# Kernel optimization log

Measured on AMD Instinct MI355X. Metric: run time of the kernel, lower is better.

The kernel has to match this reference:

```python
import jax, jax.numpy as jnp
import numpy as np

N, DIM, HEADS = 4096, 256, 4
DK = DIM // HEADS
EPS = 1e-5


def setup_inputs() -> dict:
    key = jax.random.key(0)
    ks = jax.random.split(key, 12)
    x = jax.random.normal(ks[0], (N, DIM), dtype=jnp.float32)
    adj = (jax.random.uniform(ks[1], (N, N)) < 0.05).astype(jnp.float32)
    s = 1.0 / np.sqrt(DIM).astype(np.float32)
    Wq = jax.random.normal(ks[2], (DIM, DIM), dtype=jnp.float32) * s
    bq = jnp.zeros((DIM,), jnp.float32)
    Wk = jax.random.normal(ks[3], (DIM, DIM), dtype=jnp.float32) * s
    bk = jnp.zeros((DIM,), jnp.float32)
    Wv = jax.random.normal(ks[4], (DIM, DIM), dtype=jnp.float32) * s
    bv = jnp.zeros((DIM,), jnp.float32)
    Wo = jax.random.normal(ks[5], (DIM, DIM), dtype=jnp.float32) * s
    bo = jnp.zeros((DIM,), jnp.float32)
    gamma = jnp.ones((DIM,), jnp.float32)
    beta = jnp.zeros((DIM,), jnp.float32)
    return {"x": x, "adj": adj, "Wq": Wq, "bq": bq, "Wk": Wk, "bk": bk,
            "Wv": Wv, "bv": bv, "Wo": Wo, "bo": bo, "gamma": gamma, "beta": beta}


def reference(x, adj, Wq, bq, Wk, bk, Wv, bv, Wo, bo, gamma, beta):
    n = x.shape[0]
    # projections -> [N, H, dk]
    Q = (x @ Wq.T + bq).reshape(n, HEADS, DK)
    K = (x @ Wk.T + bk).reshape(n, HEADS, DK)
    V = (x @ Wv.T + bv).reshape(n, HEADS, DK)
    inv_sqrt_dk = jnp.asarray(1.0 / np.sqrt(DK), x.dtype)
    # [N, N, H] scores, multiplicative adjacency mask BEFORE softmax
    scores = jnp.einsum('ihd,jhd->ijh', Q, K) * inv_sqrt_dk
    scores = scores * adj[:, :, None]
    weights = jax.nn.softmax(scores, axis=1)  # softmax over source nodes j
    out = jnp.einsum('ijh,jhd->ihd', weights, V).reshape(n, DIM)
    out = out @ Wo.T + bo
    # residual + LayerNorm
    h = out + x
    mu = jnp.mean(h, axis=-1, keepdims=True)
    var = jnp.mean(jnp.square(h - mu), axis=-1, keepdims=True)
    return (h - mu) * jax.lax.rsqrt(var + EPS) * gamma + beta
```

## Files before the change

### kernel.cpp

```cpp
#include <hip/hip_runtime.h>
#include <math.h>

#define NN 4096
#define ECAP 768

typedef float f32x4 __attribute__((ext_vector_type(4)));

__device__ __forceinline__ float bf2f(unsigned short u) {
    union { unsigned int i; float f; } c; c.i = ((unsigned int)u) << 16; return c.f;
}
__device__ __forceinline__ unsigned short f2bf(float f) {
    union { float f; unsigned int i; } c; c.f = f;
    const unsigned int r = c.i + 0x7FFFu + ((c.i >> 16) & 1u);
    return (unsigned short)(r >> 16);
}

__global__ __launch_bounds__(256) void qkv_gemm(
    const float* __restrict__ x,
    const float* __restrict__ Wq, const float* __restrict__ Wk, const float* __restrict__ Wv,
    const float* __restrict__ bq, const float* __restrict__ bk, const float* __restrict__ bv,
    float* __restrict__ Q, unsigned short* __restrict__ Kb, unsigned short* __restrict__ Vb,
    float* __restrict__ S)
{
    __shared__ float As[32][68];
    __shared__ float Bs[32][68];

    const int which = blockIdx.z;
    const float* __restrict__ W    = which == 0 ? Wq : (which == 1 ? Wk : Wv);
    const float* __restrict__ bias = which == 0 ? bq : (which == 1 ? bk : bv);

    const int tid = threadIdx.x;
    const int tx = tid & 15, ty = tid >> 4;
    const int row0 = blockIdx.x * 64, col0 = blockIdx.y * 64;
    const int lr = tid >> 3;
    const int lc = (tid & 7) * 4;

    float acc[4][4] = {};

    for (int k0 = 0; k0 < 256; k0 += 32) {
        const float4 a0 = *(const float4*)(x + (size_t)(row0 + lr) * 256 + k0 + lc);
        const float4 a1 = *(const float4*)(x + (size_t)(row0 + lr + 32) * 256 + k0 + lc);
        const float4 w0 = *(const float4*)(W + (size_t)(col0 + lr) * 256 + k0 + lc);
        const float4 w1 = *(const float4*)(W + (size_t)(col0 + lr + 32) * 256 + k0 + lc);
        __syncthreads();
        As[lc + 0][lr] = a0.x; As[lc + 1][lr] = a0.y; As[lc + 2][lr] = a0.z; As[lc + 3][lr] = a0.w;
        As[lc + 0][lr + 32] = a1.x; As[lc + 1][lr + 32] = a1.y; As[lc + 2][lr + 32] = a1.z; As[lc + 3][lr + 32] = a1.w;
        Bs[lc + 0][lr] = w0.x; Bs[lc + 1][lr] = w0.y; Bs[lc + 2][lr] = w0.z; Bs[lc + 3][lr] = w0.w;
        Bs[lc + 0][lr + 32] = w1.x; Bs[lc + 1][lr + 32] = w1.y; Bs[lc + 2][lr + 32] = w1.z; Bs[lc + 3][lr + 32] = w1.w;
        __syncthreads();
#pragma unroll
        for (int kk = 0; kk < 32; kk++) {
            const float4 av = *(const float4*)&As[kk][ty * 4];
            const float4 bv4 = *(const float4*)&Bs[kk][tx * 4];
            acc[0][0] = fmaf(av.x, bv4.x, acc[0][0]); acc[0][1] = fmaf(av.x, bv4.y, acc[0][1]);
            acc[0][2] = fmaf(av.x, bv4.z, acc[0][2]); acc[0][3] = fmaf(av.x, bv4.w, acc[0][3]);
            acc[1][0] = fmaf(av.y, bv4.x, acc[1][0]); acc[1][1] = fmaf(av.y, bv4.y, acc[1][1]);
            acc[1][2] = fmaf(av.y, bv4.z, acc[1][2]); acc[1][3] = fmaf(av.y, bv4.w, acc[1][3]);
            acc[2][0] = fmaf(av.z, bv4.x, acc[2][0]); acc[2][1] = fmaf(av.z, bv4.y, acc[2][1]);
            acc[2][2] = fmaf(av.z, bv4.z, acc[2][2]); acc[2][3] = fmaf(av.z, bv4.w, acc[2][3]);
            acc[3][0] = fmaf(av.w, bv4.x, acc[3][0]); acc[3][1] = fmaf(av.w, bv4.y, acc[3][1]);
            acc[3][2] = fmaf(av.w, bv4.z, acc[3][2]); acc[3][3] = fmaf(av.w, bv4.w, acc[3][3]);
        }
    }

    const int gc = col0 + tx * 4;
    const float4 b4 = *(const float4*)(bias + gc);
    float cs0 = 0.f, cs1 = 0.f, cs2 = 0.f, cs3 = 0.f;
#pragma unroll
    for (int r = 0; r < 4; r++) {
        const int gr = row0 + ty * 4 + r;
        float4 v;
        v.x = acc[r][0] + b4.x; v.y = acc[r][1] + b4.y;
        v.z = acc[r][2] + b4.z; v.w = acc[r][3] + b4.w;
        if (which == 0) {
            *(float4*)(Q + (size_t)gr * 256 + gc) = v;
        } else {
            ushort4 pk;
            pk.x = f2bf(v.x); pk.y = f2bf(v.y); pk.z = f2bf(v.z); pk.w = f2bf(v.w);
            *(ushort4*)((which == 1 ? Kb : Vb) + (size_t)gr * 256 + gc) = pk;
            cs0 += v.x; cs1 += v.y; cs2 += v.z; cs3 += v.w;
        }
    }
    if (which == 2) {
        __syncthreads();
        float* red = &As[0][0];
        red[ty * 68 + tx * 4 + 0] = cs0;
        red[ty * 68 + tx * 4 + 1] = cs1;
        red[ty * 68 + tx * 4 + 2] = cs2;
        red[ty * 68 + tx * 4 + 3] = cs3;
        __syncthreads();
        if (ty == 0) {
#pragma unroll
            for (int c = 0; c < 4; c++) {
                float s = 0.f;
#pragma unroll
                for (int t = 0; t < 16; t++) s += red[t * 68 + tx * 4 + c];
                atomicAdd(&S[gc + c], s);
            }
        }
    }
}

__global__ __launch_bounds__(512, 4) void attn_v4(
    const float* __restrict__ Q, const unsigned short* __restrict__ K,
    const unsigned short* __restrict__ V, const float* __restrict__ adj,
    const float* __restrict__ S, float* __restrict__ out)
{
    __shared__ unsigned short lj[ECAP];
    __shared__ float wgt[ECAP * 4];
    __shared__ float pnum[2][256];
    __shared__ float pden[2][4];
    __shared__ int wtot[8], wbase[8], cnt;

    const int i = blockIdx.x;
    const int tid = threadIdx.x;
    const int wave = tid >> 6;
    const int lane = tid & 63;

    const f32x4* __restrict__ arow = (const f32x4*)(adj + (size_t)i * NN);
    const f32x4 a0 = __builtin_nontemporal_load(arow + 2 * tid);
    const f32x4 a1 = __builtin_nontemporal_load(arow + 2 * tid + 1);
    const int c = (a0.x != 0.f) + (a0.y != 0.f) + (a0.z != 0.f) + (a0.w != 0.f)
                + (a1.x != 0.f) + (a1.y != 0.f) + (a1.z != 0.f) + (a1.w != 0.f);
    int incl = c;
#pragma unroll
    for (int s = 1; s < 64; s <<= 1) {
        const int v = __shfl_up(incl, s);
        if (lane >= s) incl += v;
    }
    if (lane == 63) wtot[wave] = incl;
    __syncthreads();
    if (tid == 0) {
        int s = 0;
#pragma unroll
        for (int w = 0; w < 8; w++) { wbase[w] = s; s += wtot[w]; }
        cnt = s;
    }
    __syncthreads();
    {
        int p = wbase[wave] + incl - c;
        const int j0 = tid * 8;
        if (a0.x != 0.f && p < ECAP) lj[p++] = (unsigned short)(j0 + 0);
        if (a0.y != 0.f && p < ECAP) lj[p++] = (unsigned short)(j0 + 1);
        if (a0.z != 0.f && p < ECAP) lj[p++] = (unsigned short)(j0 + 2);
        if (a0.w != 0.f && p < ECAP) lj[p++] = (unsigned short)(j0 + 3);
        if (a1.x != 0.f && p < ECAP) lj[p++] = (unsigned short)(j0 + 4);
        if (a1.y != 0.f && p < ECAP) lj[p++] = (unsigned short)(j0 + 5);
        if (a1.z != 0.f && p < ECAP) lj[p++] = (unsigned short)(j0 + 6);
        if (a1.w != 0.f && p < ECAP) lj[p++] = (unsigned short)(j0 + 7);
    }
    __syncthreads();
    const int m = min(cnt, ECAP);

    const float4 qraw = ((const float4*)(Q + (size_t)i * 256))[lane];
    const float QS = 0.125f * 1.44269504089f;
    const float4 qv = {qraw.x * QS, qraw.y * QS, qraw.z * QS, qraw.w * QS};
    for (int e0 = wave * 4; e0 < m; e0 += 32) {
        int jj[4];
#pragma unroll
        for (int u = 0; u < 4; u++)
            jj[u] = (e0 + u < m) ? (int)lj[e0 + u] : (int)lj[e0];
        ushort4 kv[4];
#pragma unroll
        for (int u = 0; u < 4; u++)
            kv[u] = ((const ushort4*)(K + (size_t)jj[u] * 256))[lane];
#pragma unroll
        for (int u = 0; u < 4; u++) {
            float d = bf2f(kv[u].x) * qv.x + bf2f(kv[u].y) * qv.y
                    + bf2f(kv[u].z) * qv.z + bf2f(kv[u].w) * qv.w;
            d += __shfl_xor(d, 1);
            d += __shfl_xor(d, 2);
            d += __shfl_xor(d, 4);
            d += __shfl_xor(d, 8);
            if ((lane & 15) == 0 && e0 + u < m)
                wgt[(e0 + u) * 4 + (lane >> 4)] = exp2f(d) - 1.f;
        }
    }
    __syncthreads();

    const int g = tid >> 8;
    const int d = tid & 255;
    const int head = d >> 6;
    float num = 0.f, den = 0.f;
    int e = g;
    for (; e + 14 < m; e += 16) {
        float w[8];
#pragma unroll
        for (int u = 0; u < 8; u++) w[u] = wgt[(e + 2 * u) * 4 + head];
        float v[8];
#pragma unroll
        for (int u = 0; u < 8; u++)
            v[u] = bf2f(V[(size_t)lj[e + 2 * u] * 256 + d]);
#pragma unroll
        for (int u = 0; u < 8; u++) { num = fmaf(w[u], v[u], num); den += w[u]; }
    }
    for (; e < m; e += 2) {
        const float w = wgt[e * 4 + head];
        num = fmaf(w, bf2f(V[(size_t)lj[e] * 256 + d]), num);
        den += w;
    }
    pnum[g][d] = num;
    if ((d & 63) == 0) pden[g][head] = den;
    __syncthreads();

    if (tid < 256) {
        const int h = tid >> 6;
        const float dn = pden[0][h] + pden[1][h] + 4096.0f;
        out[(size_t)i * 256 + tid] = (pnum[0][tid] + pnum[1][tid] + S[tid]) / dn;
    }
}

__global__ __launch_bounds__(256) void out_gemm(
    const float* __restrict__ A, const float* __restrict__ Wo,
    const float* __restrict__ bo, const float* __restrict__ x,
    float* __restrict__ H)
{
    __shared__ float As[32][68];
    __shared__ float Bs[32][68];
    const int tid = threadIdx.x;
    const int tx = tid & 15, ty = tid >> 4;
    const int row0 = blockIdx.x * 64, col0 = blockIdx.y * 64;
    const int lr = tid >> 3;
    const int lc = (tid & 7) * 4;

    float acc[4][4] = {};

    for (int k0 = 0; k0 < 256; k0 += 32) {
        const float4 a0 = *(const float4*)(A + (size_t)(row0 + lr) * 256 + k0 + lc);
        const float4 a1 = *(const float4*)(A + (size_t)(row0 + lr + 32) * 256 + k0 + lc);
        const float4 w0 = *(const float4*)(Wo + (size_t)(col0 + lr) * 256 + k0 + lc);
        const float4 w1 = *(const float4*)(Wo + (size_t)(col0 + lr + 32) * 256 + k0 + lc);
        __syncthreads();
        As[lc + 0][lr] = a0.x; As[lc + 1][lr] = a0.y; As[lc + 2][lr] = a0.z; As[lc + 3][lr] = a0.w;
        As[lc + 0][lr + 32] = a1.x; As[lc + 1][lr + 32] = a1.y; As[lc + 2][lr + 32] = a1.z; As[lc + 3][lr + 32] = a1.w;
        Bs[lc + 0][lr] = w0.x; Bs[lc + 1][lr] = w0.y; Bs[lc + 2][lr] = w0.z; Bs[lc + 3][lr] = w0.w;
        Bs[lc + 0][lr + 32] = w1.x; Bs[lc + 1][lr + 32] = w1.y; Bs[lc + 2][lr + 32] = w1.z; Bs[lc + 3][lr + 32] = w1.w;
        __syncthreads();
#pragma unroll
        for (int kk = 0; kk < 32; kk++) {
            const float4 av = *(const float4*)&As[kk][ty * 4];
            const float4 bv4 = *(const float4*)&Bs[kk][tx * 4];
            acc[0][0] = fmaf(av.x, bv4.x, acc[0][0]); acc[0][1] = fmaf(av.x, bv4.y, acc[0][1]);
            acc[0][2] = fmaf(av.x, bv4.z, acc[0][2]); acc[0][3] = fmaf(av.x, bv4.w, acc[0][3]);
            acc[1][0] = fmaf(av.y, bv4.x, acc[1][0]); acc[1][1] = fmaf(av.y, bv4.y, acc[1][1]);
            acc[1][2] = fmaf(av.y, bv4.z, acc[1][2]); acc[1][3] = fmaf(av.y, bv4.w, acc[1][3]);
            acc[2][0] = fmaf(av.z, bv4.x, acc[2][0]); acc[2][1] = fmaf(av.z, bv4.y, acc[2][1]);
            acc[2][2] = fmaf(av.z, bv4.z, acc[2][2]); acc[2][3] = fmaf(av.z, bv4.w, acc[2][3]);
            acc[3][0] = fmaf(av.w, bv4.x, acc[3][0]); acc[3][1] = fmaf(av.w, bv4.y, acc[3][1]);
            acc[3][2] = fmaf(av.w, bv4.z, acc[3][2]); acc[3][3] = fmaf(av.w, bv4.w, acc[3][3]);
        }
    }
#pragma unroll
    for (int r = 0; r < 4; r++) {
        const int gr = row0 + ty * 4 + r;
        const int gc = col0 + tx * 4;
        const float4 rv = *(const float4*)(x + (size_t)gr * 256 + gc);
        float4 v;
        v.x = acc[r][0] + bo[gc + 0] + rv.x;
        v.y = acc[r][1] + bo[gc + 1] + rv.y;
        v.z = acc[r][2] + bo[gc + 2] + rv.z;
        v.w = acc[r][3] + bo[gc + 3] + rv.w;
        *(float4*)(H + (size_t)gr * 256 + gc) = v;
    }
}

__global__ __launch_bounds__(256) void ln_kernel(
    const float* __restrict__ H, const float* __restrict__ gamma,
    const float* __restrict__ beta, float* __restrict__ out)
{
    const int row = blockIdx.x * 4 + (threadIdx.x >> 6);
    const int lane = threadIdx.x & 63;
    const float4 v = ((const float4*)(H + (size_t)row * 256))[lane];
    float s = (v.x + v.y) + (v.z + v.w);
#pragma unroll
    for (int o = 1; o < 64; o <<= 1) s += __shfl_xor(s, o);
    const float mu = s * (1.f / 256.f);
    const float dx = v.x - mu, dy = v.y - mu, dz = v.z - mu, dw = v.w - mu;
    float sq = (dx * dx + dy * dy) + (dz * dz + dw * dw);
#pragma unroll
    for (int o = 1; o < 64; o <<= 1) sq += __shfl_xor(sq, o);
    const float rstd = rsqrtf(sq * (1.f / 256.f) + 1e-5f);
    const float4 g = ((const float4*)gamma)[lane];
    const float4 b = ((const float4*)beta)[lane];
    float4 o4;
    o4.x = dx * rstd * g.x + b.x;
    o4.y = dy * rstd * g.y + b.y;
    o4.z = dz * rstd * g.z + b.z;
    o4.w = dw * rstd * g.w + b.w;
    ((float4*)(out + (size_t)row * 256))[lane] = o4;
}

extern "C" void kernel_launch(void* const* d_in, const int* in_sizes, int n_in,
                              void* d_out, int out_size, void* d_ws, size_t ws_size,
                              hipStream_t stream)
{
    const float* x     = (const float*)d_in[0];
    const float* adj   = (const float*)d_in[1];
    const float* Wq    = (const float*)d_in[2];
    const float* bq    = (const float*)d_in[3];
    const float* Wk    = (const float*)d_in[4];
    const float* bk    = (const float*)d_in[5];
    const float* Wv    = (const float*)d_in[6];
    const float* bv    = (const float*)d_in[7];
    const float* Wo    = (const float*)d_in[8];
    const float* bo    = (const float*)d_in[9];
    const float* gamma = (const float*)d_in[10];
    const float* beta  = (const float*)d_in[11];

    float* ws = (float*)d_ws;
    const size_t NM = (size_t)NN * 256;
    float* Qb          = ws;
    unsigned short* Kb = (unsigned short*)(ws + NM);
    unsigned short* Vb = Kb + NM;
    float* AT          = ws + 2 * NM;
    float* H           = ws + 3 * NM;
    float* S           = ws + 4 * NM;

    (void)hipMemsetAsync(S, 0, 256 * sizeof(float), stream);
    qkv_gemm<<<dim3(64, 4, 3), 256, 0, stream>>>(x, Wq, Wk, Wv, bq, bk, bv, Qb, Kb, Vb, S);
    attn_v4<<<NN, 512, 0, stream>>>(Qb, Kb, Vb, adj, S, AT);
    out_gemm<<<dim3(64, 4), 256, 0, stream>>>(AT, Wo, bo, x, H);
    ln_kernel<<<1024, 256, 0, stream>>>(H, gamma, beta, (float*)d_out);
}
```

Measured before the change: 248.1 us.

## Enlarge QKV GEMM tiles and pad edge lists to restructure attention gather

```diff
diff --git a/kernel.cpp b/kernel.cpp
--- a/kernel.cpp
+++ b/kernel.cpp
@@ -13,6 +13,10 @@
     union { float f; unsigned int i; } c; c.f = f;
     const unsigned int r = c.i + 0x7FFFu + ((c.i >> 16) & 1u);
     return (unsigned short)(r >> 16);
+}
+
+__device__ __forceinline__ int bswz(int col) {
+    return col ^ (((col >> 5) & 3) << 2);
 }
 
 __global__ __launch_bounds__(256) void qkv_gemm(
@@ -22,94 +26,108 @@
     float* __restrict__ Q, unsigned short* __restrict__ Kb, unsigned short* __restrict__ Vb,
     float* __restrict__ S)
 {
-    __shared__ float As[32][68];
-    __shared__ float Bs[32][68];
+    __shared__ float As[32][132];
+    __shared__ float Bs[32][132];
 
     const int which = blockIdx.z;
     const float* __restrict__ W    = which == 0 ? Wq : (which == 1 ? Wk : Wv);
     const float* __restrict__ bias = which == 0 ? bq : (which == 1 ? bk : bv);
 
     const int tid = threadIdx.x;
-    const int tx = tid & 15, ty = tid >> 4;
-    const int row0 = blockIdx.x * 64, col0 = blockIdx.y * 64;
-    const int lr = tid >> 3;
-    const int lc = (tid & 7) * 4;
-
-    float acc[4][4] = {};
+    const int row0 = blockIdx.x * 128, col0 = blockIdx.y * 128;
+    const int lr = tid >> 1;
+    const int lk = (tid & 1) * 16;
+    const int ty = tid >> 4, tx = tid & 15;
+    const int lrs = bswz(lr);
+
+    float acc[8][8] = {};
 
     for (int k0 = 0; k0 < 256; k0 += 32) {
-        const float4 a0 = *(const float4*)(x + (size_t)(row0 + lr) * 256 + k0 + lc);
-        const float4 a1 = *(const float4*)(x + (size_t)(row0 + lr + 32) * 256 + k0 + lc);
-        const float4 w0 = *(const float4*)(W + (size_t)(col0 + lr) * 256 + k0 + lc);
-        const float4 w1 = *(const float4*)(W + (size_t)(col0 + lr + 32) * 256 + k0 + lc);
-        __syncthreads();
-        As[lc + 0][lr] = a0.x; As[lc + 1][lr] = a0.y; As[lc + 2][lr] = a0.z; As[lc + 3][lr] = a0.w;
-        As[lc + 0][lr + 32] = a1.x; As[lc + 1][lr + 32] = a1.y; As[lc + 2][lr + 32] = a1.z; As[lc + 3][lr + 32] = a1.w;
-        Bs[lc + 0][lr] = w0.x; Bs[lc + 1][lr] = w0.y; Bs[lc + 2][lr] = w0.z; Bs[lc + 3][lr] = w0.w;
-        Bs[lc + 0][lr + 32] = w1.x; Bs[lc + 1][lr + 32] = w1.y; Bs[lc + 2][lr + 32] = w1.z; Bs[lc + 3][lr + 32] = w1.w;
+        float4 a[4], b[4];
+#pragma unroll
+        for (int j = 0; j < 4; j++) {
+            a[j] = *(const float4*)(x + (size_t)(row0 + lr) * 256 + k0 + lk + 4 * j);
+            b[j] = *(const float4*)(W + (size_t)(col0 + lr) * 256 + k0 + lk + 4 * j);
+        }
+        __syncthreads();
+#pragma unroll
+        for (int j = 0; j < 4; j++) {
+            As[lk + 4 * j + 0][lr] = a[j].x; As[lk + 4 * j + 1][lr] = a[j].y;
+            As[lk + 4 * j + 2][lr] = a[j].z; As[lk + 4 * j + 3][lr] = a[j].w;
+            Bs[lk + 4 * j + 0][lrs] = b[j].x; Bs[lk + 4 * j + 1][lrs] = b[j].y;
+            Bs[lk + 4 * j + 2][lrs] = b[j].z; Bs[lk + 4 * j + 3][lrs] = b[j].w;
+        }
         __syncthreads();
 #pragma unroll
         for (int kk = 0; kk < 32; kk++) {
-            const float4 av = *(const float4*)&As[kk][ty * 4];
-            const float4 bv4 = *(const float4*)&Bs[kk][tx * 4];
-            acc[0][0] = fmaf(av.x, bv4.x, acc[0][0]); acc[0][1] = fmaf(av.x, bv4.y, acc[0][1]);
-            acc[0][2] = fmaf(av.x, bv4.z, acc[0][2]); acc[0][3] = fmaf(av.x, bv4.w, acc[0][3]);
-            acc[1][0] = fmaf(av.y, bv4.x, acc[1][0]); acc[1][1] = fmaf(av.y, bv4.y, acc[1][1]);
-            acc[1][2] = fmaf(av.y, bv4.z, acc[1][2]); acc[1][3] = fmaf(av.y, bv4.w, acc[1][3]);
-            acc[2][0] = fmaf(av.z, bv4.x, acc[2][0]); acc[2][1] = fmaf(av.z, bv4.y, acc[2][1]);
-            acc[2][2] = fmaf(av.z, bv4.z, acc[2][2]); acc[2][3] = fmaf(av.z, bv4.w, acc[2][3]);
-            acc[3][0] = fmaf(av.w, bv4.x, acc[3][0]); acc[3][1] = fmaf(av.w, bv4.y, acc[3][1]);
-            acc[3][2] = fmaf(av.w, bv4.z, acc[3][2]); acc[3][3] = fmaf(av.w, bv4.w, acc[3][3]);
-        }
-    }
-
-    const int gc = col0 + tx * 4;
-    const float4 b4 = *(const float4*)(bias + gc);
-    float cs0 = 0.f, cs1 = 0.f, cs2 = 0.f, cs3 = 0.f;
-#pragma unroll
-    for (int r = 0; r < 4; r++) {
-        const int gr = row0 + ty * 4 + r;
-        float4 v;
-        v.x = acc[r][0] + b4.x; v.y = acc[r][1] + b4.y;
-        v.z = acc[r][2] + b4.z; v.w = acc[r][3] + b4.w;
+            const float4 a0 = *(const float4*)&As[kk][ty * 8];
+            const float4 a1 = *(const float4*)&As[kk][ty * 8 + 4];
+            const int bc = bswz(tx * 8);
+            const float4 b0 = *(const float4*)&Bs[kk][bc];
+            const float4 b1 = *(const float4*)&Bs[kk][bc ^ 4];
+            const float av[8] = {a0.x, a0.y, a0.z, a0.w, a1.x, a1.y, a1.z, a1.w};
+            const float bw[8] = {b0.x, b0.y, b0.z, b0.w, b1.x, b1.y, b1.z, b1.w};
+#pragma unroll
+            for (int r = 0; r < 8; r++)
+#pragma unroll
+                for (int c = 0; c < 8; c++)
+                    acc[r][c] = fmaf(av[r], bw[c], acc[r][c]);
+        }
+    }
+
+    const int gc = col0 + tx * 8;
+    const float4 blo = *(const float4*)(bias + gc);
+    const float4 bhi = *(const float4*)(bias + gc + 4);
+    float cs[8] = {};
+#pragma unroll
+    for (int r = 0; r < 8; r++) {
+        const int gr = row0 + ty * 8 + r;
+        float v[8];
+        v[0] = acc[r][0] + blo.x; v[1] = acc[r][1] + blo.y;
+        v[2] = acc[r][2] + blo.z; v[3] = acc[r][3] + blo.w;
+        v[4] = acc[r][4] + bhi.x; v[5] = acc[r][5] + bhi.y;
+        v[6] = acc[r][6] + bhi.z; v[7] = acc[r][7] + bhi.w;
         if (which == 0) {
-            *(float4*)(Q + (size_t)gr * 256 + gc) = v;
+            float4 o0, o1;
+            o0.x = v[0]; o0.y = v[1]; o0.z = v[2]; o0.w = v[3];
+            o1.x = v[4]; o1.y = v[5]; o1.z = v[6]; o1.w = v[7];
+            *(float4*)(Q + (size_t)gr * 256 + gc) = o0;
+            *(float4*)(Q + (size_t)gr * 256 + gc + 4) = o1;
         } else {
-            ushort4 pk;
-            pk.x = f2bf(v.x); pk.y = f2bf(v.y); pk.z = f2bf(v.z); pk.w = f2bf(v.w);
-            *(ushort4*)((which == 1 ? Kb : Vb) + (size_t)gr * 256 + gc) = pk;
-            cs0 += v.x; cs1 += v.y; cs2 += v.z; cs3 += v.w;
+            ushort4 p0, p1;
+            p0.x = f2bf(v[0]); p0.y = f2bf(v[1]); p0.z = f2bf(v[2]); p0.w = f2bf(v[3]);
+            p1.x = f2bf(v[4]); p1.y = f2bf(v[5]); p1.z = f2bf(v[6]); p1.w = f2bf(v[7]);
+            unsigned short* C = (which == 1 ? Kb : Vb);
+            *(ushort4*)(C + (size_t)gr * 256 + gc) = p0;
+            *(ushort4*)(C + (size_t)gr * 256 + gc + 4) = p1;
+#pragma unroll
+            for (int c = 0; c < 8; c++) cs[c] += v[c];
         }
     }
     if (which == 2) {
         __syncthreads();
         float* red = &As[0][0];
-        red[ty * 68 + tx * 4 + 0] = cs0;
-        red[ty * 68 + tx * 4 + 1] = cs1;
-        red[ty * 68 + tx * 4 + 2] = cs2;
-        red[ty * 68 + tx * 4 + 3] = cs3;
-        __syncthreads();
-        if (ty == 0) {
-#pragma unroll
-            for (int c = 0; c < 4; c++) {
-                float s = 0.f;
-#pragma unroll
-                for (int t = 0; t < 16; t++) s += red[t * 68 + tx * 4 + c];
-                atomicAdd(&S[gc + c], s);
-            }
-        }
-    }
-}
-
-__global__ __launch_bounds__(512, 4) void attn_v4(
+#pragma unroll
+        for (int c = 0; c < 8; c++) red[(tx * 8 + c) * 17 + ty] = cs[c];
+        __syncthreads();
+        if (tid < 128) {
+            float s = 0.f;
+#pragma unroll
+            for (int t = 0; t < 16; t++) s += red[tid * 17 + t];
+            atomicAdd(&S[col0 + tid], s);
+        }
+    }
+}
+
+__global__ __launch_bounds__(512, 4) void attn_v5(
     const float* __restrict__ Q, const unsigned short* __restrict__ K,
     const unsigned short* __restrict__ V, const float* __restrict__ adj,
     const float* __restrict__ S, float* __restrict__ out)
 {
     __shared__ unsigned short lj[ECAP];
     __shared__ float wgt[ECAP * 4];
-    __shared__ float pnum[2][256];
-    __shared__ float pden[2][4];
+    __shared__ float pnum[4][256];
+    __shared__ float pden[4][4];
     __shared__ int wtot[8], wbase[8], cnt;
 
     const int i = blockIdx.x;
@@ -151,19 +169,23 @@
     }
     __syncthreads();
     const int m = min(cnt, ECAP);
+    const int mp = min((m + 31) & ~31, ECAP);
+    for (int e = m + tid; e < mp; e += 512) lj[e] = 0;
+    __syncthreads();
 
     const float4 qraw = ((const float4*)(Q + (size_t)i * 256))[lane];
     const float QS = 0.125f * 1.44269504089f;
     const float4 qv = {qraw.x * QS, qraw.y * QS, qraw.z * QS, qraw.w * QS};
-    for (int e0 = wave * 4; e0 < m; e0 += 32) {
-        int jj[4];
+    const unsigned lane4 = (unsigned)(lane << 2);
+    for (int e0 = wave * 4; e0 < mp; e0 += 32) {
+        unsigned off[4];
 #pragma unroll
         for (int u = 0; u < 4; u++)
-            jj[u] = (e0 + u < m) ? (int)lj[e0 + u] : (int)lj[e0];
+            off[u] = ((unsigned)lj[e0 + u] << 8) + lane4;
         ushort4 kv[4];
 #pragma unroll
         for (int u = 0; u < 4; u++)
-            kv[u] = ((const ushort4*)(K + (size_t)jj[u] * 256))[lane];
+            kv[u] = *(const ushort4*)(K + off[u]);
 #pragma unroll
         for (int u = 0; u < 4; u++) {
             float d = bf2f(kv[u].x) * qv.x + bf2f(kv[u].y) * qv.y
@@ -172,41 +194,40 @@
             d += __shfl_xor(d, 2);
             d += __shfl_xor(d, 4);
             d += __shfl_xor(d, 8);
-            if ((lane & 15) == 0 && e0 + u < m)
-                wgt[(e0 + u) * 4 + (lane >> 4)] = exp2f(d) - 1.f;
-        }
-    }
-    __syncthreads();
-
-    const int g = tid >> 8;
-    const int d = tid & 255;
-    const int head = d >> 6;
-    float num = 0.f, den = 0.f;
-    int e = g;
-    for (; e + 14 < m; e += 16) {
-        float w[8];
-#pragma unroll
-        for (int u = 0; u < 8; u++) w[u] = wgt[(e + 2 * u) * 4 + head];
-        float v[8];
-#pragma unroll
-        for (int u = 0; u < 8; u++)
-            v[u] = bf2f(V[(size_t)lj[e + 2 * u] * 256 + d]);
-#pragma unroll
-        for (int u = 0; u < 8; u++) { num = fmaf(w[u], v[u], num); den += w[u]; }
-    }
-    for (; e < m; e += 2) {
-        const float w = wgt[e * 4 + head];
-        num = fmaf(w, bf2f(V[(size_t)lj[e] * 256 + d]), num);
-        den += w;
-    }
-    pnum[g][d] = num;
-    if ((d & 63) == 0) pden[g][head] = den;
+            float w = exp2f(d) - 1.f;
+            if (e0 + u >= m) w = 0.f;
+            if ((lane & 15) == 0) wgt[(e0 + u) * 4 + (lane >> 4)] = w;
+        }
+    }
+    __syncthreads();
+
+    const int g = tid >> 7;
+    const int t = tid & 127;
+    const int d0 = t * 2;
+    const int head = t >> 5;
+    float nx = 0.f, ny = 0.f, den = 0.f;
+    for (int e = g; e < mp; e += 32) {
+#pragma unroll
+        for (int u = 0; u < 8; u++) {
+            const int ee = e + 4 * u;
+            const float w = wgt[ee * 4 + head];
+            const unsigned off = ((unsigned)lj[ee] << 8) + (unsigned)d0;
+            const ushort2 v2 = *(const ushort2*)(V + off);
+            nx = fmaf(w, bf2f(v2.x), nx);
+            ny = fmaf(w, bf2f(v2.y), ny);
+            den += w;
+        }
+    }
+    pnum[g][d0] = nx;
+    pnum[g][d0 + 1] = ny;
+    if ((t & 31) == 0) pden[g][head] = den;
     __syncthreads();
 
     if (tid < 256) {
         const int h = tid >> 6;
-        const float dn = pden[0][h] + pden[1][h] + 4096.0f;
-        out[(size_t)i * 256 + tid] = (pnum[0][tid] + pnum[1][tid] + S[tid]) / dn;
+        const float dn = (pden[0][h] + pden[1][h]) + (pden[2][h] + pden[3][h]) + 4096.0f;
+        const float nm = (pnum[0][tid] + pnum[1][tid]) + (pnum[2][tid] + pnum[3][tid]) + S[tid];
+        out[(size_t)i * 256 + tid] = nm / dn;
     }
 }
 
@@ -317,8 +338,8 @@
     float* S           = ws + 4 * NM;
 
     (void)hipMemsetAsync(S, 0, 256 * sizeof(float), stream);
-    qkv_gemm<<<dim3(64, 4, 3), 256, 0, stream>>>(x, Wq, Wk, Wv, bq, bk, bv, Qb, Kb, Vb, S);
-    attn_v4<<<NN, 512, 0, stream>>>(Qb, Kb, Vb, adj, S, AT);
+    qkv_gemm<<<dim3(32, 2, 3), 256, 0, stream>>>(x, Wq, Wk, Wv, bq, bk, bv, Qb, Kb, Vb, S);
+    attn_v5<<<NN, 512, 0, stream>>>(Qb, Kb, Vb, adj, S, AT);
     out_gemm<<<dim3(64, 4), 256, 0, stream>>>(AT, Wo, bo, x, H);
     ln_kernel<<<1024, 256, 0, stream>>>(H, gamma, beta, (float*)d_out);
 }
```

Result: faster. 238.5 us (-3.8%).
